# Kernel tuning notes

Hardware: AMD Instinct MI355X
Metric: run time of the kernel (lower is better)

Reference implementation:

```python
import jax, jax.numpy as jnp
import numpy as np

COMMITMENT_COST = 0.25
ENTROPY_LOSS_WEIGHT = 0.1
EPSILON = 1e-05
NUM_EMBEDDINGS = 2048
EMBEDDING_DIM = 64


def setup_inputs() -> dict:
    key = jax.random.key(0)
    kx, ke = jax.random.split(key)
    x = jax.random.normal(kx, (16, 64, 64, EMBEDDING_DIM), dtype=jnp.float32)
    embedding = jax.random.normal(ke, (NUM_EMBEDDINGS, EMBEDDING_DIM), dtype=jnp.float32)
    return {"x": x, "embedding": embedding}


def reference(x, embedding):
    input_shape = x.shape
    flat_x = x.reshape(-1, EMBEDDING_DIM)              # [N, D]
    distances = (jnp.sum(flat_x ** 2, axis=1, keepdims=True)
                 + jnp.sum(embedding ** 2, axis=1)
                 - 2.0 * jnp.matmul(flat_x, embedding.T))
    encoding_indices = jnp.argmin(distances, axis=1)   # [N]
    quantized = embedding[encoding_indices].reshape(input_shape)

    commitment_loss = jnp.mean((jax.lax.stop_gradient(quantized) - x) ** 2)
    codebook_loss = jnp.mean((quantized - jax.lax.stop_gradient(x)) ** 2)
    # straight-through estimator
    quantized = x + jax.lax.stop_gradient(quantized - x)

    # histogram of code usage == mean of one-hot encodings (scatter-add, avoids [N,K] one-hot)
    n_tokens = flat_x.shape[0]
    counts = jnp.zeros((NUM_EMBEDDINGS,), dtype=flat_x.dtype).at[encoding_indices].add(1.0)
    avg_probs = counts / n_tokens
    perplexity = jnp.exp(-jnp.sum(avg_probs * jnp.log(avg_probs + EPSILON)))
    entropy_loss = jnp.sum(avg_probs * jnp.log(avg_probs + EPSILON))

    vq_loss = codebook_loss + COMMITMENT_COST * commitment_loss + ENTROPY_LOSS_WEIGHT * entropy_loss
    return (quantized, vq_loss, commitment_loss, codebook_loss, perplexity,
            entropy_loss, encoding_indices.reshape(input_shape[:-1]), avg_probs)
```

## Files before the change

kernel.cpp:

```cpp
#include <hip/hip_runtime.h>
#include <float.h>

typedef _Float16 half8 __attribute__((ext_vector_type(8)));
typedef float    f32x4 __attribute__((ext_vector_type(4)));

constexpr int N_TOK = 65536;
constexpr int D     = 64;
constexpr int K     = 2048;
constexpr int TILE_C = 64;
constexpr int NTILE  = K / TILE_C;
constexpr int TOK_PER_BLK = 64;
constexpr int NBLK = N_TOK / TOK_PER_BLK;
constexpr float EPS_RESCORE = 2e-3f;

constexpr size_t QN       = (size_t)N_TOK * D;
constexpr size_t SCAL_OFF = QN;
constexpr size_t IDX_OFF  = QN + 5;
constexpr size_t PROB_OFF = IDX_OFF + N_TOK;

constexpr size_t WS_HNORM = 0;
constexpr size_t WS_COUNT = 8192;
constexpr size_t WS_BSUM  = 16384;
constexpr size_t WS_SW    = 24576;
constexpr int REC_B  = 80;
constexpr int TILE_B = 256 * REC_B;

__device__ inline unsigned long long pack_key(float d, int k) {
    unsigned u = __float_as_uint(d);
    u = (u & 0x80000000u) ? ~u : (u | 0x80000000u);
    return ((unsigned long long)u << 32) | (unsigned)k;
}

__device__ inline float unpack_dist(unsigned long long key) {
    unsigned u = (unsigned)(key >> 32);
    u = (u & 0x80000000u) ? (u & 0x7FFFFFFFu) : ~u;
    return __uint_as_float(u);
}

__device__ inline unsigned long long shfl_xor_u64_w16(unsigned long long v, int m) {
    int lo = __shfl_xor((int)(unsigned)v, m, 16);
    int hi = __shfl_xor((int)(unsigned)(v >> 32), m, 16);
    return ((unsigned long long)(unsigned)hi << 32) | (unsigned)lo;
}

__global__ __launch_bounds__(256) void vq_init(const float* __restrict__ emb,
                                               float* __restrict__ hnorm,
                                               unsigned* __restrict__ counts,
                                               double* __restrict__ blocksums,
                                               char* __restrict__ swb) {
    const int g  = blockIdx.x * 256 + threadIdx.x;
    const int r  = g >> 3;
    const int c0 = g & 7;
    const float4* p4 = (const float4*)(emb + (size_t)r * D + 8 * c0);
    float4 q0 = p4[0], q1 = p4[1];
    float v[8] = {q0.x, q0.y, q0.z, q0.w, q1.x, q1.y, q1.z, q1.w};
    half8 h, l;
    float s = 0.f;
#pragma unroll
    for (int i = 0; i < 8; ++i) {
        s += v[i] * v[i];
        _Float16 hh = (_Float16)v[i];
        h[i] = hh;
        l[i] = (_Float16)(v[i] - (float)hh);
    }
    const int t    = r >> 6;
    const int w    = (r >> 4) & 3;
    const int m16  = r & 15;
    const int lane = (c0 & 3) * 16 + m16;
    const int slot = c0 >> 2;
    char* rec = swb + (size_t)(t * 256 + w * 64 + lane) * REC_B;
    *(half8*)(rec + slot * 16)       = h;
    *(half8*)(rec + (2 + slot) * 16) = l;

#pragma unroll
    for (int off = 1; off < 8; off <<= 1) s += __shfl_xor(s, off, 8);
    if (c0 < 4) *(float*)(rec + 64) = 0.5f * s;
    if (c0 == 0) hnorm[r] = 0.5f * s;
    if (g < K) counts[g] = 0u;
    if (g < NBLK) blocksums[g] = 0.0;
}

#define ISSUE(P0, P1, P2, P3, HN)                                                  \
  {                                                                                \
    asm volatile("global_load_dwordx4 %0, %5, off\n\t"                             \
                 "global_load_dwordx4 %1, %5, off offset:16\n\t"                   \
                 "global_load_dwordx4 %2, %5, off offset:32\n\t"                   \
                 "global_load_dwordx4 %3, %5, off offset:48\n\t"                   \
                 "global_load_dword   %4, %5, off offset:64"                       \
                 : "=&v"(P0), "=&v"(P1), "=&v"(P2), "=&v"(P3), "=&v"(HN)           \
                 : "v"(pl));                                                       \
    pl += TILE_B;                                                                  \
  }

#define WAITC(N)                                                                   \
  asm volatile("s_waitcnt vmcnt(" #N ")" ::: "memory");                            \
  __builtin_amdgcn_sched_barrier(0);

#define VQ_STEP(P0, P1, P2, P3, HN, TT)                                            \
  {                                                                                \
    f32x4 acc[4];                                                                  \
    __builtin_amdgcn_s_setprio(1);                                                 \
    _Pragma("unroll")                                                              \
    for (int a = 0; a < 4; ++a) {                                                  \
      acc[a] = (f32x4){(HN), (HN), (HN), (HN)};                                    \
      acc[a] = __builtin_amdgcn_mfma_f32_16x16x32_f16(axh[a][0], P0, acc[a], 0, 0, 0); \
      acc[a] = __builtin_amdgcn_mfma_f32_16x16x32_f16(axh[a][1], P1, acc[a], 0, 0, 0); \
      acc[a] = __builtin_amdgcn_mfma_f32_16x16x32_f16(axl[a][0], P0, acc[a], 0, 0, 0); \
      acc[a] = __builtin_amdgcn_mfma_f32_16x16x32_f16(axl[a][1], P1, acc[a], 0, 0, 0); \
      acc[a] = __builtin_amdgcn_mfma_f32_16x16x32_f16(axh[a][0], P2, acc[a], 0, 0, 0); \
      acc[a] = __builtin_amdgcn_mfma_f32_16x16x32_f16(axh[a][1], P3, acc[a], 0, 0, 0); \
    }                                                                              \
    __builtin_amdgcn_s_setprio(0);                                                 \
    _Pragma("unroll")                                                              \
    for (int a = 0; a < 4; ++a)                                                    \
      _Pragma("unroll")                                                            \
      for (int r = 0; r < 4; ++r) {                                                \
        unsigned _kb = (__float_as_uint(acc[a][r]) & 0xFFFFFFE0u) | (unsigned)(TT);\
        best_d[a][r] = fminf(best_d[a][r], __uint_as_float(_kb));                  \
      }                                                                            \
  }

__global__ __launch_bounds__(256, 2) void vq_fused(const float* __restrict__ x,
                                                   const float* __restrict__ emb,
                                                   const float* __restrict__ hnorm,
                                                   const char* __restrict__ swb,
                                                   unsigned* __restrict__ counts,
                                                   double* __restrict__ blocksums,
                                                   float* __restrict__ out) {
    __shared__ unsigned long long kls[64][5];
    __shared__ int bks[64];
    __shared__ double wsum[4];

    const int tid  = threadIdx.x;
    const int lane = tid & 63;
    const int wav  = tid >> 6;
    const int t0   = blockIdx.x * TOK_PER_BLK;
    const int m16  = lane & 15;
    const int g    = lane >> 4;
    const int ko   = g * 8;
    const int cit  = wav * 16 + m16;

    half8 axh[4][2], axl[4][2];
#pragma unroll
    for (int a = 0; a < 4; ++a) {
        const float* xr = x + (size_t)(t0 + 16 * a + m16) * D;
#pragma unroll
        for (int c = 0; c < 2; ++c) {
            const float4* p4 = (const float4*)(xr + 32 * c + ko);
            float4 q0 = p4[0], q1 = p4[1];
            float v[8] = {q0.x, q0.y, q0.z, q0.w, q1.x, q1.y, q1.z, q1.w};
            half8 h, l;
#pragma unroll
            for (int j = 0; j < 8; ++j) {
                float nv = -v[j];
                _Float16 hh = (_Float16)nv;
                h[j] = hh;
                l[j] = (_Float16)(nv - (float)hh);
            }
            axh[a][c] = h; axl[a][c] = l;
        }
    }

    float best_d[4][4];
#pragma unroll
    for (int a = 0; a < 4; ++a)
#pragma unroll
        for (int r = 0; r < 4; ++r) best_d[a][r] = FLT_MAX;

    const char* pl = swb + (size_t)tid * REC_B;

    half8 A0, A1, A2, A3;  float hA;
    half8 B0, B1, B2, B3;  float hB;
    half8 C0, C1, C2, C3;  float hC;

    ISSUE(A0, A1, A2, A3, hA);
    ISSUE(B0, B1, B2, B3, hB);

    for (int t = 0; t < 28; t += 3) {
        ISSUE(C0, C1, C2, C3, hC);
        WAITC(10);
        VQ_STEP(A0, A1, A2, A3, hA, t);
        ISSUE(A0, A1, A2, A3, hA);
        WAITC(10);
        VQ_STEP(B0, B1, B2, B3, hB, t + 1);
        ISSUE(B0, B1, B2, B3, hB);
        WAITC(10);
        VQ_STEP(C0, C1, C2, C3, hC, t + 2);
    }
    WAITC(5);
    VQ_STEP(A0, A1, A2, A3, hA, 30);
    WAITC(0);
    VQ_STEP(B0, B1, B2, B3, hB, 31);

#pragma unroll
    for (int a = 0; a < 4; ++a)
#pragma unroll
        for (int r = 0; r < 4; ++r) {
            const unsigned bits = __float_as_uint(best_d[a][r]);
            const int code = (int)(bits & 31u) * TILE_C + cit;
            unsigned long long key = pack_key(best_d[a][r], code);
#pragma unroll
            for (int off = 8; off; off >>= 1) {
                unsigned long long o = shfl_xor_u64_w16(key, off);
                if (o < key) key = o;
            }
            if (m16 == 0) kls[16 * a + g * 4 + r][wav] = key;
        }
    __syncthreads();

    if (tid < 64) {
        float ds[4]; int kk[4];
        unsigned long long kmin = ~0ULL;
#pragma unroll
        for (int w = 0; w < 4; ++w) {
            unsigned long long key = kls[tid][w];
            ds[w] = unpack_dist(key);
            kk[w] = (int)(unsigned)(key & 0xFFFFFFFFu);
            if (key < kmin) kmin = key;
        }
        int bk = (int)(unsigned)(kmin & 0xFFFFFFFFu);
        const float fmin = unpack_dist(kmin);
        int cnt = 0;
#pragma unroll
        for (int w = 0; w < 4; ++w) cnt += (ds[w] <= fmin + EPS_RESCORE) ? 1 : 0;

        if (cnt > 1) {
            unsigned long long bkey = ~0ULL;
            const float* xr = x + (size_t)(t0 + tid) * D;
            for (int w = 0; w < 4; ++w) {
                if (ds[w] <= fmin + EPS_RESCORE) {
                    const int k = kk[w];
                    const float* cr = emb + (size_t)k * D;
                    float s0 = 0.f, s1 = 0.f, s2 = 0.f, s3 = 0.f;
#pragma unroll
                    for (int i = 0; i < 16; ++i) {
                        s0 = fmaf(cr[4 * i + 0], xr[4 * i + 0], s0);
                        s1 = fmaf(cr[4 * i + 1], xr[4 * i + 1], s1);
                        s2 = fmaf(cr[4 * i + 2], xr[4 * i + 2], s2);
                        s3 = fmaf(cr[4 * i + 3], xr[4 * i + 3], s3);
                    }
                    float hd = hnorm[k] - ((s0 + s1) + (s2 + s3));
                    unsigned long long key = pack_key(hd, k);
                    if (key < bkey) bkey = key;
                }
            }
            bk = (int)(unsigned)(bkey & 0xFFFFFFFFu);
        }
        bks[tid] = bk;
        out[IDX_OFF + t0 + tid] = (float)bk;
        atomicAdd(&counts[bk], 1u);
    }
    __syncthreads();

    const int tok = tid >> 2;
    const int i4  = tid & 3;
    const int bk  = bks[tok];
    const float4* xr4 = (const float4*)(x + (size_t)(t0 + tok) * D);
    const float4* cr4 = (const float4*)(emb + (size_t)bk * D);
    float4* qr4 = (float4*)(out + (size_t)(t0 + tok) * D);
    float local = 0.f;
#pragma unroll
    for (int ii = 0; ii < 4; ++ii) {
        const int idx = i4 + 4 * ii;
        float4 xv = xr4[idx];
        float4 cv = cr4[idx];
        float dx = cv.x - xv.x, dy = cv.y - xv.y;
        float dz = cv.z - xv.z, dw = cv.w - xv.w;
        local += dx * dx + dy * dy + dz * dz + dw * dw;
        float4 q;
        q.x = xv.x + dx; q.y = xv.y + dy;
        q.z = xv.z + dz; q.w = xv.w + dw;
        qr4[idx] = q;
    }
    double ld = (double)local;
#pragma unroll
    for (int off = 32; off > 0; off >>= 1) ld += __shfl_down(ld, off, 64);
    if (lane == 0) wsum[wav] = ld;
    __syncthreads();
    if (tid == 0)
        blocksums[blockIdx.x] = (wsum[0] + wsum[1]) + (wsum[2] + wsum[3]);
}

__global__ __launch_bounds__(256) void vq_finalize(const unsigned* __restrict__ counts,
                                                   const double* __restrict__ blocksums,
                                                   float* __restrict__ out) {
    const int tid = threadIdx.x;
    double e = 0.0;
#pragma unroll
    for (int i = 0; i < 8; ++i) {
        int k = tid + i * 256;
        float p = (float)counts[k] / 65536.0f;
        out[PROB_OFF + k] = p;
        double pd = (double)p;
        e += pd * log(pd + 1e-5);
    }
    double s = 0.0;
#pragma unroll
    for (int i = 0; i < NBLK / 256; ++i) s += blocksums[tid + i * 256];
#pragma unroll
    for (int off = 32; off > 0; off >>= 1) {
        e += __shfl_down(e, off, 64);
        s += __shfl_down(s, off, 64);
    }
    __shared__ double we[4], ws2[4];
    int lane = tid & 63, wid = tid >> 6;
    if (lane == 0) { we[wid] = e; ws2[wid] = s; }
    __syncthreads();
    if (tid == 0) {
        double entropy = (we[0] + we[1]) + (we[2] + we[3]);
        double sumsq   = (ws2[0] + ws2[1]) + (ws2[2] + ws2[3]);
        double mse     = sumsq / (double)((size_t)N_TOK * D);
        out[SCAL_OFF + 0] = (float)(1.25 * mse + 0.1 * entropy);
        out[SCAL_OFF + 1] = (float)mse;
        out[SCAL_OFF + 2] = (float)mse;
        out[SCAL_OFF + 3] = (float)exp(-entropy);
        out[SCAL_OFF + 4] = (float)entropy;
    }
}

extern "C" void kernel_launch(void* const* d_in, const int* in_sizes, int n_in,
                              void* d_out, int out_size, void* d_ws, size_t ws_size,
                              hipStream_t stream) {
    const float* x   = (const float*)d_in[0];
    const float* emb = (const float*)d_in[1];
    float* out = (float*)d_out;

    char* ws = (char*)d_ws;
    float*    hnorm     = (float*)(ws + WS_HNORM);
    unsigned* counts    = (unsigned*)(ws + WS_COUNT);
    double*   blocksums = (double*)(ws + WS_BSUM);
    char*     swb       = ws + WS_SW;

    vq_init<<<K * 8 / 256, 256, 0, stream>>>(emb, hnorm, counts, blocksums, swb);
    vq_fused<<<NBLK, 256, 0, stream>>>(x, emb, hnorm, swb, counts, blocksums, out);
    vq_finalize<<<1, 256, 0, stream>>>(counts, blocksums, out);
}
```

Measured before the change: 132.5 us.

## Drop split-fp16 compensation, track top-2 candidates and widen exact rescoring

The distance matmul now uses a single fp16 product per element instead of the hi/lo split. This cuts the MFMA count from six to two per tile and halves the codebook records streamed from memory. To make up for the lost accuracy, each lane keeps its best two candidates, the cross-lane reduction merges top-2 lists, and the rescoring margin is widened so more near-ties are recomputed exactly in fp32. The risk is more rescoring work in the epilogue, and a wrong argmin if the true nearest code falls outside the top-2 per column group.

```diff
diff --git a/kernel.cpp b/kernel.cpp
--- a/kernel.cpp
+++ b/kernel.cpp
@@ -11,7 +11,7 @@
 constexpr int NTILE  = K / TILE_C;
 constexpr int TOK_PER_BLK = 64;
 constexpr int NBLK = N_TOK / TOK_PER_BLK;
-constexpr float EPS_RESCORE = 2e-3f;
+constexpr float EPS_RESCORE = 0.15f;
 
 constexpr size_t QN       = (size_t)N_TOK * D;
 constexpr size_t SCAL_OFF = QN;
@@ -22,7 +22,7 @@
 constexpr size_t WS_COUNT = 8192;
 constexpr size_t WS_BSUM  = 16384;
 constexpr size_t WS_SW    = 24576;
-constexpr int REC_B  = 80;
+constexpr int REC_B  = 40;
 constexpr int TILE_B = 256 * REC_B;
 
 __device__ inline unsigned long long pack_key(float d, int k) {
@@ -54,14 +54,12 @@
     const float4* p4 = (const float4*)(emb + (size_t)r * D + 8 * c0);
     float4 q0 = p4[0], q1 = p4[1];
     float v[8] = {q0.x, q0.y, q0.z, q0.w, q1.x, q1.y, q1.z, q1.w};
-    half8 h, l;
+    half8 h;
     float s = 0.f;
 #pragma unroll
     for (int i = 0; i < 8; ++i) {
         s += v[i] * v[i];
-        _Float16 hh = (_Float16)v[i];
-        h[i] = hh;
-        l[i] = (_Float16)(v[i] - (float)hh);
+        h[i] = (_Float16)v[i];
     }
     const int t    = r >> 6;
     const int w    = (r >> 4) & 3;
@@ -69,25 +67,22 @@
     const int lane = (c0 & 3) * 16 + m16;
     const int slot = c0 >> 2;
     char* rec = swb + (size_t)(t * 256 + w * 64 + lane) * REC_B;
-    *(half8*)(rec + slot * 16)       = h;
-    *(half8*)(rec + (2 + slot) * 16) = l;
+    *(half8*)(rec + slot * 16) = h;
 
 #pragma unroll
     for (int off = 1; off < 8; off <<= 1) s += __shfl_xor(s, off, 8);
-    if (c0 < 4) *(float*)(rec + 64) = 0.5f * s;
+    if (c0 < 4) *(float*)(rec + 32) = 0.5f * s;
     if (c0 == 0) hnorm[r] = 0.5f * s;
     if (g < K) counts[g] = 0u;
     if (g < NBLK) blocksums[g] = 0.0;
 }
 
-#define ISSUE(P0, P1, P2, P3, HN)                                                  \
+#define ISSUE(P0, P1, HN)                                                          \
   {                                                                                \
-    asm volatile("global_load_dwordx4 %0, %5, off\n\t"                             \
-                 "global_load_dwordx4 %1, %5, off offset:16\n\t"                   \
-                 "global_load_dwordx4 %2, %5, off offset:32\n\t"                   \
-                 "global_load_dwordx4 %3, %5, off offset:48\n\t"                   \
-                 "global_load_dword   %4, %5, off offset:64"                       \
-                 : "=&v"(P0), "=&v"(P1), "=&v"(P2), "=&v"(P3), "=&v"(HN)           \
+    asm volatile("global_load_dwordx4 %0, %3, off\n\t"                             \
+                 "global_load_dwordx4 %1, %3, off offset:16\n\t"                   \
+                 "global_load_dword   %2, %3, off offset:32"                       \
+                 : "=&v"(P0), "=&v"(P1), "=&v"(HN)                                 \
                  : "v"(pl));                                                       \
     pl += TILE_B;                                                                  \
   }
@@ -96,7 +91,7 @@
   asm volatile("s_waitcnt vmcnt(" #N ")" ::: "memory");                            \
   __builtin_amdgcn_sched_barrier(0);
 
-#define VQ_STEP(P0, P1, P2, P3, HN, TT)                                            \
+#define VQ_STEP(P0, P1, HN, TT)                                                    \
   {                                                                                \
     f32x4 acc[4];                                                                  \
     __builtin_amdgcn_s_setprio(1);                                                 \
@@ -105,10 +100,6 @@
       acc[a] = (f32x4){(HN), (HN), (HN), (HN)};                                    \
       acc[a] = __builtin_amdgcn_mfma_f32_16x16x32_f16(axh[a][0], P0, acc[a], 0, 0, 0); \
       acc[a] = __builtin_amdgcn_mfma_f32_16x16x32_f16(axh[a][1], P1, acc[a], 0, 0, 0); \
-      acc[a] = __builtin_amdgcn_mfma_f32_16x16x32_f16(axl[a][0], P0, acc[a], 0, 0, 0); \
-      acc[a] = __builtin_amdgcn_mfma_f32_16x16x32_f16(axl[a][1], P1, acc[a], 0, 0, 0); \
-      acc[a] = __builtin_amdgcn_mfma_f32_16x16x32_f16(axh[a][0], P2, acc[a], 0, 0, 0); \
-      acc[a] = __builtin_amdgcn_mfma_f32_16x16x32_f16(axh[a][1], P3, acc[a], 0, 0, 0); \
     }                                                                              \
     __builtin_amdgcn_s_setprio(0);                                                 \
     _Pragma("unroll")                                                              \
@@ -116,7 +107,9 @@
       _Pragma("unroll")                                                            \
       for (int r = 0; r < 4; ++r) {                                                \
         unsigned _kb = (__float_as_uint(acc[a][r]) & 0xFFFFFFE0u) | (unsigned)(TT);\
-        best_d[a][r] = fminf(best_d[a][r], __uint_as_float(_kb));                  \
+        float _f = __uint_as_float(_kb);                                           \
+        best2[a][r] = fminf(best2[a][r], fmaxf(best1[a][r], _f));                  \
+        best1[a][r] = fminf(best1[a][r], _f);                                      \
       }                                                                            \
   }
 
@@ -127,7 +120,7 @@
                                                    unsigned* __restrict__ counts,
                                                    double* __restrict__ blocksums,
                                                    float* __restrict__ out) {
-    __shared__ unsigned long long kls[64][5];
+    __shared__ unsigned long long kls[64][10];
     __shared__ int bks[64];
     __shared__ double wsum[4];
 
@@ -140,7 +133,7 @@
     const int ko   = g * 8;
     const int cit  = wav * 16 + m16;
 
-    half8 axh[4][2], axl[4][2];
+    half8 axh[4][2];
 #pragma unroll
     for (int a = 0; a < 4; ++a) {
         const float* xr = x + (size_t)(t0 + 16 * a + m16) * D;
@@ -149,70 +142,73 @@
             const float4* p4 = (const float4*)(xr + 32 * c + ko);
             float4 q0 = p4[0], q1 = p4[1];
             float v[8] = {q0.x, q0.y, q0.z, q0.w, q1.x, q1.y, q1.z, q1.w};
-            half8 h, l;
-#pragma unroll
-            for (int j = 0; j < 8; ++j) {
-                float nv = -v[j];
-                _Float16 hh = (_Float16)nv;
-                h[j] = hh;
-                l[j] = (_Float16)(nv - (float)hh);
+            half8 h;
+#pragma unroll
+            for (int j = 0; j < 8; ++j) h[j] = (_Float16)(-v[j]);
+            axh[a][c] = h;
+        }
+    }
+
+    float best1[4][4], best2[4][4];
+#pragma unroll
+    for (int a = 0; a < 4; ++a)
+#pragma unroll
+        for (int r = 0; r < 4; ++r) { best1[a][r] = FLT_MAX; best2[a][r] = FLT_MAX; }
+
+    const char* pl = swb + (size_t)tid * REC_B;
+
+    half8 A0, A1;  float hA;
+    half8 B0, B1;  float hB;
+    half8 C0, C1;  float hC;
+
+    ISSUE(A0, A1, hA);
+    ISSUE(B0, B1, hB);
+
+    for (int t = 0; t < 28; t += 3) {
+        ISSUE(C0, C1, hC);
+        WAITC(6);
+        VQ_STEP(A0, A1, hA, t);
+        ISSUE(A0, A1, hA);
+        WAITC(6);
+        VQ_STEP(B0, B1, hB, t + 1);
+        ISSUE(B0, B1, hB);
+        WAITC(6);
+        VQ_STEP(C0, C1, hC, t + 2);
+    }
+    WAITC(3);
+    VQ_STEP(A0, A1, hA, 30);
+    WAITC(0);
+    VQ_STEP(B0, B1, hB, 31);
+
+#pragma unroll
+    for (int a = 0; a < 4; ++a)
+#pragma unroll
+        for (int r = 0; r < 4; ++r) {
+            const unsigned b1 = __float_as_uint(best1[a][r]);
+            const unsigned b2 = __float_as_uint(best2[a][r]);
+            unsigned long long k1 = pack_key(best1[a][r], (int)(b1 & 31u) * TILE_C + cit);
+            unsigned long long k2 = pack_key(best2[a][r], (int)(b2 & 31u) * TILE_C + cit);
+#pragma unroll
+            for (int off = 8; off; off >>= 1) {
+                unsigned long long o1 = shfl_xor_u64_w16(k1, off);
+                unsigned long long o2 = shfl_xor_u64_w16(k2, off);
+                unsigned long long hi1 = (k1 > o1) ? k1 : o1;
+                unsigned long long lo2 = (k2 < o2) ? k2 : o2;
+                k1 = (k1 < o1) ? k1 : o1;
+                k2 = (hi1 < lo2) ? hi1 : lo2;
             }
-            axh[a][c] = h; axl[a][c] = l;
-        }
-    }
-
-    float best_d[4][4];
-#pragma unroll
-    for (int a = 0; a < 4; ++a)
-#pragma unroll
-        for (int r = 0; r < 4; ++r) best_d[a][r] = FLT_MAX;
-
-    const char* pl = swb + (size_t)tid * REC_B;
-
-    half8 A0, A1, A2, A3;  float hA;
-    half8 B0, B1, B2, B3;  float hB;
-    half8 C0, C1, C2, C3;  float hC;
-
-    ISSUE(A0, A1, A2, A3, hA);
-    ISSUE(B0, B1, B2, B3, hB);
-
-    for (int t = 0; t < 28; t += 3) {
-        ISSUE(C0, C1, C2, C3, hC);
-        WAITC(10);
-        VQ_STEP(A0, A1, A2, A3, hA, t);
-        ISSUE(A0, A1, A2, A3, hA);
-        WAITC(10);
-        VQ_STEP(B0, B1, B2, B3, hB, t + 1);
-        ISSUE(B0, B1, B2, B3, hB);
-        WAITC(10);
-        VQ_STEP(C0, C1, C2, C3, hC, t + 2);
-    }
-    WAITC(5);
-    VQ_STEP(A0, A1, A2, A3, hA, 30);
-    WAITC(0);
-    VQ_STEP(B0, B1, B2, B3, hB, 31);
-
-#pragma unroll
-    for (int a = 0; a < 4; ++a)
-#pragma unroll
-        for (int r = 0; r < 4; ++r) {
-            const unsigned bits = __float_as_uint(best_d[a][r]);
-            const int code = (int)(bits & 31u) * TILE_C + cit;
-            unsigned long long key = pack_key(best_d[a][r], code);
-#pragma unroll
-            for (int off = 8; off; off >>= 1) {
-                unsigned long long o = shfl_xor_u64_w16(key, off);
-                if (o < key) key = o;
+            if (m16 == 0) {
+                kls[16 * a + g * 4 + r][wav]     = k1;
+                kls[16 * a + g * 4 + r][4 + wav] = k2;
             }
-            if (m16 == 0) kls[16 * a + g * 4 + r][wav] = key;
         }
     __syncthreads();
 
     if (tid < 64) {
-        float ds[4]; int kk[4];
+        float ds[8]; int kk[8];
         unsigned long long kmin = ~0ULL;
 #pragma unroll
-        for (int w = 0; w < 4; ++w) {
+        for (int w = 0; w < 8; ++w) {
             unsigned long long key = kls[tid][w];
             ds[w] = unpack_dist(key);
             kk[w] = (int)(unsigned)(key & 0xFFFFFFFFu);
@@ -222,12 +218,12 @@
         const float fmin = unpack_dist(kmin);
         int cnt = 0;
 #pragma unroll
-        for (int w = 0; w < 4; ++w) cnt += (ds[w] <= fmin + EPS_RESCORE) ? 1 : 0;
+        for (int w = 0; w < 8; ++w) cnt += (ds[w] <= fmin + EPS_RESCORE) ? 1 : 0;
 
         if (cnt > 1) {
             unsigned long long bkey = ~0ULL;
             const float* xr = x + (size_t)(t0 + tid) * D;
-            for (int w = 0; w < 4; ++w) {
+            for (int w = 0; w < 8; ++w) {
                 if (ds[w] <= fmin + EPS_RESCORE) {
                     const int k = kk[w];
                     const float* cr = emb + (size_t)k * D;
```

Result: no change. 130.6 us (-1.5%).
